# Kernel optimization log

Hardware: AMD Instinct MI355X
Metric: run time of the kernel (lower is better)

Reference implementation:

```python
import jax, jax.numpy as jnp
import numpy as np

B, T, D = 2, 2048, 2048
H, KV, DH = 16, 8, 128
N, W, K = 1024, 256, 8


def rotate_half(x):
    x1, x2 = x[..., : DH // 2], x[..., DH // 2 :]
    return jnp.concatenate((-x2, x1), axis=-1)


def setup_inputs() -> dict:
    key = jax.random.key(0)
    ks = jax.random.split(key, 10)
    hidden_states = jax.random.normal(ks[0], (B, T, D), dtype=jnp.float32)
    cos = jax.random.uniform(ks[1], (B, T, DH), dtype=jnp.float32, minval=-1.0, maxval=1.0)
    sin = jax.random.uniform(ks[2], (B, T, DH), dtype=jnp.float32, minval=-1.0, maxval=1.0)
    mem = jax.random.normal(ks[3], (B, N, D), dtype=jnp.float32)
    Wq = jax.random.normal(ks[4], (D, D), dtype=jnp.float32) * 0.02
    Wk = jax.random.normal(ks[5], (KV * DH, D), dtype=jnp.float32) * 0.02
    Wv = jax.random.normal(ks[6], (KV * DH, D), dtype=jnp.float32) * 0.02
    Wo = jax.random.normal(ks[7], (D, D), dtype=jnp.float32) * 0.02
    Wg = jnp.zeros((1, D), dtype=jnp.float32)          # module inits gate weight to zeros
    bg = jnp.full((1,), 2.0, dtype=jnp.float32)        # and gate bias to 2.0
    return dict(hidden_states=hidden_states, cos=cos, sin=sin, mem=mem,
                Wq=Wq, Wk=Wk, Wv=Wv, Wo=Wo, Wg=Wg, bg=bg)


def reference(hidden_states, cos, sin, mem, Wq, Wk, Wv, Wo, Wg, bg):
    scale = DH ** -0.5
    n_rep = H // KV
    # projections -> [B, heads, T, d_h]
    q = (hidden_states @ Wq.T).reshape(B, T, H, DH).transpose(0, 2, 1, 3)
    k = (hidden_states @ Wk.T).reshape(B, T, KV, DH).transpose(0, 2, 1, 3)
    v = (hidden_states @ Wv.T).reshape(B, T, KV, DH).transpose(0, 2, 1, 3)
    # rotary (cos/sin are [B,T,d_h] -> broadcast over heads)
    c, s = cos[:, None], sin[:, None]
    q = q * c + rotate_half(q) * s
    k = k * c + rotate_half(k) * s
    # GQA repeat kv heads
    k_local = jnp.repeat(k, n_rep, axis=1)
    v_local = jnp.repeat(v, n_rep, axis=1)
    # --- local sliding-window causal attention (dense TxT mask, as in SDPA path) ---
    row = jnp.arange(T)[:, None]
    col = jnp.arange(T)[None, :]
    allowed = (col <= row) & (col >= row - W + 1)
    bias = jnp.where(allowed, 0.0, -jnp.inf).astype(q.dtype)
    scores = jnp.einsum('bhtd,bhsd->bhts', q, k_local) * scale + bias
    o_local = jnp.einsum('bhts,bhsd->bhtd', jax.nn.softmax(scores, axis=-1), v_local)
    o_local = o_local.transpose(0, 2, 1, 3).reshape(B, T, D) @ Wo.T
    # --- memory retrieval path (memory is detached in the original) ---
    mem_c = jax.lax.stop_gradient(mem)
    k_mem = (mem_c @ Wk.T).reshape(B, N, KV, DH).transpose(0, 2, 1, 3)
    v_mem = (mem_c @ Wv.T).reshape(B, N, KV, DH).transpose(0, 2, 1, 3)
    k_mem = jnp.repeat(k_mem, n_rep, axis=1)  # [B,H,N,d_h]
    v_mem = jnp.repeat(v_mem, n_rep, axis=1)
    q_chunk = q.mean(axis=2)                  # [B,H,d_h]
    sim_chunk = jnp.einsum('bhd,bhnd->bhn', q_chunk, k_mem) * scale
    _, idx = jax.lax.top_k(sim_chunk, K)      # [B,H,K]
    k_sh = jnp.take_along_axis(k_mem, idx[..., None], axis=2)  # [B,H,K,d_h]
    v_sh = jnp.take_along_axis(v_mem, idx[..., None], axis=2)
    sim_tok = jnp.einsum('bhtd,bhkd->bhtk', q, k_sh) * scale
    o_mem = jnp.einsum('bhtk,bhkd->bhtd', jax.nn.softmax(sim_tok, axis=-1), v_sh)
    o_mem = o_mem.transpose(0, 2, 1, 3).reshape(B, T, D)
    # --- learned gate fusion ---
    g = jax.nn.sigmoid(hidden_states @ Wg.T + bg)  # [B,T,1]
    return g * o_local + (1.0 - g) * o_mem
```

## Files before the change

kernel.cpp:

```cpp
#include <hip/hip_runtime.h>
#include <stdint.h>

#define B_   2
#define T_   2048
#define D_   2048
#define H_   16
#define KV_  8
#define DH_  128
#define NMEM 1024
#define WWIN 256
#define KSEL 8
#define BT   (B_*T_)
#define KVSTR 2048
#define QKVSTR 4096

__constant__ const float kScale = 0.08838834764831845f;

typedef __attribute__((ext_vector_type(8))) short s16x8;
typedef __attribute__((ext_vector_type(4))) float f32x4;

__device__ inline unsigned short f2bf(float f) {
  union { float f; unsigned int u; } c; c.f = f;
  unsigned int u = c.u;
  unsigned int r = u + 0x7fffu + ((u >> 16) & 1u);
  return (unsigned short)(r >> 16);
}
__device__ inline float bf2f(unsigned short v) {
  union { unsigned int u; float f; } c; c.u = ((unsigned int)v) << 16;
  return c.f;
}
__device__ inline f32x4 fzero4() { f32x4 v; v[0]=0.f; v[1]=0.f; v[2]=0.f; v[3]=0.f; return v; }

__global__ __launch_bounds__(256) void conv_kernel(const float* __restrict__ src,
                                                   unsigned short* __restrict__ dst, int n) {
  int i = blockIdx.x * 256 + threadIdx.x;
  if (i * 4 >= n) return;
  float4 v = ((const float4*)src)[i];
  uint2 o;
  o.x = (unsigned)f2bf(v.x) | ((unsigned)f2bf(v.y) << 16);
  o.y = (unsigned)f2bf(v.z) | ((unsigned)f2bf(v.w) << 16);
  ((uint2*)dst)[i] = o;
}

#define AOFF(buf, half) ((buf)*32768 + (half)*16384)
#define BOFF(buf, half) (65536 + (buf)*32768 + (half)*16384)

#define PH_MFMA(P, BF) \
  { \
    _Pragma("unroll") \
    for (int mi = 0; mi < 2; ++mi) { \
      _Pragma("unroll") \
      for (int ni = 0; ni < 4; ++ni) { \
        acc[P][mi][ni] = __builtin_amdgcn_mfma_f32_16x16x32_bf16(af[mi][0], BF[ni][0], acc[P][mi][ni], 0, 0, 0); \
        acc[P][mi][ni] = __builtin_amdgcn_mfma_f32_16x16x32_bf16(af[mi][1], BF[ni][1], acc[P][mi][ni], 0, 0, 0); \
      } \
    } \
  }

template<int MODE>
__global__ __launch_bounds__(512, 2) void gemm256(const unsigned short* __restrict__ A,
                                                  const unsigned short* __restrict__ Bw,
                                                  int N, int K, int lda, int ldc,
                                                  unsigned short* __restrict__ Cb,
                                                  const float* __restrict__ g,
                                                  const unsigned short* __restrict__ omem,
                                                  float* __restrict__ dout) {
  __shared__ __align__(16) char lds[131072];
  const int tid = threadIdx.x;
  const int wv = tid >> 6, lane = tid & 63;
  const int l15 = lane & 15, lg = lane >> 4;
  const int wr = wv >> 1, wc = wv & 1;
  const int gx = gridDim.x;
  const int nwg = gx * gridDim.y;
  const int flat = blockIdx.y * gx + blockIdx.x;
  const int chunk = nwg >> 3;
  const int wg = (flat & 7) * chunk + (flat >> 3);
  const int bx = wg % gx, by = wg / gx;
  const int m0 = by * 256, n0 = bx * 256;
  const int NT = K >> 6;

  auto stage_half = [&](const unsigned short* base, int stride, int row0, int koff, int ldsoff) {
#pragma unroll
    for (int ld = 0; ld < 2; ++ld) {
      int s = ld * 512 + tid;
      int row = s >> 3, cs = s & 7;
      int cg = cs ^ (row & 7);
      const unsigned short* src = base + (size_t)(row0 + row) * stride + koff + cg * 8;
      __builtin_amdgcn_global_load_lds((const __attribute__((address_space(1))) void*)src,
          (__attribute__((address_space(3))) void*)(lds + ldsoff + ld * 8192 + wv * 1024), 16, 0, 0);
    }
  };
  auto rdA = [&](int buf, int half, int mi, int kk) -> s16x8 {
    int r = wr * 32 + mi * 16 + l15;
    int slot = (kk * 4 + lg) ^ (r & 7);
    return *(const s16x8*)(lds + AOFF(buf, half) + r * 128 + slot * 16);
  };
  auto rdB = [&](int buf, int half, int ni, int kk) -> s16x8 {
    int r = wc * 64 + ni * 16 + l15;
    int slot = (kk * 4 + lg) ^ (r & 7);
    return *(const s16x8*)(lds + BOFF(buf, half) + r * 128 + slot * 16);
  };

  f32x4 acc[4][2][4];
#pragma unroll
  for (int p = 0; p < 4; ++p)
#pragma unroll
    for (int mi = 0; mi < 2; ++mi)
#pragma unroll
      for (int ni = 0; ni < 4; ++ni) acc[p][mi][ni] = fzero4();

  stage_half(A,  lda, m0,       0,  AOFF(0, 0));
  stage_half(Bw, K,   n0,       0,  BOFF(0, 0));
  stage_half(A,  lda, m0 + 128, 0,  AOFF(0, 1));
  stage_half(Bw, K,   n0 + 128, 0,  BOFF(0, 1));
  stage_half(A,  lda, m0,       64, AOFF(1, 0));
  stage_half(Bw, K,   n0,       64, BOFF(1, 0));
  stage_half(A,  lda, m0 + 128, 64, AOFF(1, 1));
  asm volatile("s_waitcnt vmcnt(6)" ::: "memory");
  __builtin_amdgcn_s_barrier();

  int cur = 0;
  for (int t = 0; t < NT; ++t, cur ^= 1) {
    const int nxt = cur ^ 1;
    s16x8 af[2][2], b0f[4][2], b1f[4][2];
#pragma unroll
    for (int mi = 0; mi < 2; ++mi) {
      af[mi][0] = rdA(cur, 0, mi, 0);
      af[mi][1] = rdA(cur, 0, mi, 1);
    }
#pragma unroll
    for (int ni = 0; ni < 4; ++ni) {
      b0f[ni][0] = rdB(cur, 0, ni, 0);
      b0f[ni][1] = rdB(cur, 0, ni, 1);
    }
    if (t + 1 < NT) stage_half(Bw, K, n0 + 128, (t + 1) * 64, BOFF(nxt, 1));
    __builtin_amdgcn_s_barrier();
    asm volatile("s_waitcnt lgkmcnt(0)" ::: "memory");
    __builtin_amdgcn_s_setprio(1);
    PH_MFMA(0, b0f);
    __builtin_amdgcn_s_setprio(0);
    __builtin_amdgcn_s_barrier();
#pragma unroll
    for (int ni = 0; ni < 4; ++ni) {
      b1f[ni][0] = rdB(cur, 1, ni, 0);
      b1f[ni][1] = rdB(cur, 1, ni, 1);
    }
    if (t + 2 < NT) stage_half(A, lda, m0, (t + 2) * 64, AOFF(cur, 0));
    __builtin_amdgcn_s_barrier();
    asm volatile("s_waitcnt lgkmcnt(0)" ::: "memory");
    __builtin_amdgcn_s_setprio(1);
    PH_MFMA(1, b1f);
    __builtin_amdgcn_s_setprio(0);
    __builtin_amdgcn_s_barrier();
#pragma unroll
    for (int mi = 0; mi < 2; ++mi) {
      af[mi][0] = rdA(cur, 1, mi, 0);
      af[mi][1] = rdA(cur, 1, mi, 1);
    }
    if (t + 2 < NT) stage_half(Bw, K, n0, (t + 2) * 64, BOFF(cur, 0));
    __builtin_amdgcn_s_barrier();
    asm volatile("s_waitcnt lgkmcnt(0)" ::: "memory");
    __builtin_amdgcn_s_setprio(1);
    PH_MFMA(2, b0f);
    __builtin_amdgcn_s_setprio(0);
    __builtin_amdgcn_s_barrier();
    if (t + 2 < NT) stage_half(A, lda, m0 + 128, (t + 2) * 64, AOFF(cur, 1));
    __builtin_amdgcn_s_barrier();
    asm volatile("s_waitcnt lgkmcnt(0)" ::: "memory");
    __builtin_amdgcn_s_setprio(1);
    PH_MFMA(3, b1f);
    __builtin_amdgcn_s_setprio(0);
    if (t < NT - 2) asm volatile("s_waitcnt vmcnt(6)" ::: "memory");
    else            asm volatile("s_waitcnt vmcnt(0)" ::: "memory");
    __builtin_amdgcn_s_barrier();
  }

#pragma unroll
  for (int p = 0; p < 4; ++p)
#pragma unroll
    for (int mi = 0; mi < 2; ++mi)
#pragma unroll
      for (int ni = 0; ni < 4; ++ni)
#pragma unroll
        for (int j = 0; j < 4; ++j) {
          int row_g = m0 + (p >> 1) * 128 + wr * 32 + mi * 16 + lg * 4 + j;
          int col_g = n0 + (p & 1) * 128 + wc * 64 + ni * 16 + l15;
          float v = acc[p][mi][ni][j];
          size_t o = (size_t)row_g * ldc + col_g;
          if constexpr (MODE == 0) {
            Cb[o] = f2bf(v);
          } else {
            float gv = g[row_g];
            dout[o] = gv * v + (1.f - gv) * bf2f(omem[o]);
          }
        }
}

#define B2OFF(buf) (65536 + (buf)*16384)

__global__ __launch_bounds__(512, 2) void gemm256n(const unsigned short* __restrict__ A,
                                                   const unsigned short* __restrict__ Bw,
                                                   int N, int K, int lda, int ldc,
                                                   const float* __restrict__ g,
                                                   const unsigned short* __restrict__ omem,
                                                   float* __restrict__ dout) {
  __shared__ __align__(16) char lds[98304];
  const int tid = threadIdx.x;
  const int wv = tid >> 6, lane = tid & 63;
  const int l15 = lane & 15, lg = lane >> 4;
  const int wr = wv >> 1, wc = wv & 1;
  const int gx = gridDim.x;
  const int nwg = gx * gridDim.y;
  const int flat = blockIdx.y * gx + blockIdx.x;
  const int chunk = nwg >> 3;
  const int wg = (flat & 7) * chunk + (flat >> 3);
  const int bx = wg % gx, by = wg / gx;
  const int m0 = by * 256, n0 = bx * 128;
  const int NT = K >> 6;

  auto stage_half = [&](const unsigned short* base, int stride, int row0, int koff, int ldsoff) {
#pragma unroll
    for (int ld = 0; ld < 2; ++ld) {
      int s = ld * 512 + tid;
      int row = s >> 3, cs = s & 7;
      int cg = cs ^ (row & 7);
      const unsigned short* src = base + (size_t)(row0 + row) * stride + koff + cg * 8;
      __builtin_amdgcn_global_load_lds((const __attribute__((address_space(1))) void*)src,
          (__attribute__((address_space(3))) void*)(lds + ldsoff + ld * 8192 + wv * 1024), 16, 0, 0);
    }
  };
  auto rdA = [&](int buf, int half, int mi, int kk) -> s16x8 {
    int r = wr * 32 + mi * 16 + l15;
    int slot = (kk * 4 + lg) ^ (r & 7);
    return *(const s16x8*)(lds + AOFF(buf, half) + r * 128 + slot * 16);
  };
  auto rdB = [&](int buf, int ni, int kk) -> s16x8 {
    int r = wc * 64 + ni * 16 + l15;
    int slot = (kk * 4 + lg) ^ (r & 7);
    return *(const s16x8*)(lds + B2OFF(buf) + r * 128 + slot * 16);
  };

  f32x4 acc[2][2][4];
#pragma unroll
  for (int p = 0; p < 2; ++p)
#pragma unroll
    for (int mi = 0; mi < 2; ++mi)
#pragma unroll
      for (int ni = 0; ni < 4; ++ni) acc[p][mi][ni] = fzero4();

  stage_half(A,  lda, m0,       0,  AOFF(0, 0));
  stage_half(Bw, K,   n0,       0,  B2OFF(0));
  stage_half(A,  lda, m0 + 128, 0,  AOFF(0, 1));
  stage_half(A,  lda, m0,       64, AOFF(1, 0));
  stage_half(Bw, K,   n0,       64, B2OFF(1));
  asm volatile("s_waitcnt vmcnt(4)" ::: "memory");
  __builtin_amdgcn_s_barrier();

  int cur = 0;
  for (int t = 0; t < NT; ++t, cur ^= 1) {
    const int nxt = cur ^ 1;
    s16x8 af[2][2], b0f[4][2];
#pragma unroll
    for (int mi = 0; mi < 2; ++mi) {
      af[mi][0] = rdA(cur, 0, mi, 0);
      af[mi][1] = rdA(cur, 0, mi, 1);
    }
#pragma unroll
    for (int ni = 0; ni < 4; ++ni) {
      b0f[ni][0] = rdB(cur, ni, 0);
      b0f[ni][1] = rdB(cur, ni, 1);
    }
    if (t + 1 < NT) stage_half(A, lda, m0 + 128, (t + 1) * 64, AOFF(nxt, 1));
    __builtin_amdgcn_s_barrier();
    asm volatile("s_waitcnt lgkmcnt(0)" ::: "memory");
    __builtin_amdgcn_s_setprio(1);
    PH_MFMA(0, b0f);
    __builtin_amdgcn_s_setprio(0);
    __builtin_amdgcn_s_barrier();
#pragma unroll
    for (int mi = 0; mi < 2; ++mi) {
      af[mi][0] = rdA(cur, 1, mi, 0);
      af[mi][1] = rdA(cur, 1, mi, 1);
    }
    if (t + 2 < NT) {
      stage_half(A,  lda, m0, (t + 2) * 64, AOFF(cur, 0));
      stage_half(Bw, K,   n0, (t + 2) * 64, B2OFF(cur));
    }
    __builtin_amdgcn_s_barrier();
    asm volatile("s_waitcnt lgkmcnt(0)" ::: "memory");
    __builtin_amdgcn_s_setprio(1);
    PH_MFMA(1, b0f);
    __builtin_amdgcn_s_setprio(0);
    if (t < NT - 2) asm volatile("s_waitcnt vmcnt(4)" ::: "memory");
    else            asm volatile("s_waitcnt vmcnt(0)" ::: "memory");
    __builtin_amdgcn_s_barrier();
  }

#pragma unroll
  for (int p = 0; p < 2; ++p)
#pragma unroll
    for (int mi = 0; mi < 2; ++mi)
#pragma unroll
      for (int ni = 0; ni < 4; ++ni)
#pragma unroll
        for (int j = 0; j < 4; ++j) {
          int row_g = m0 + p * 128 + wr * 32 + mi * 16 + lg * 4 + j;
          int col_g = n0 + wc * 64 + ni * 16 + l15;
          float v = acc[p][mi][ni][j];
          size_t o = (size_t)row_g * ldc + col_g;
          float gv = g[row_g];
          dout[o] = gv * v + (1.f - gv) * bf2f(omem[o]);
        }
}

template<int MODE>
__global__ __launch_bounds__(256) void gemm_bt(const unsigned short* __restrict__ A,
                                               const unsigned short* __restrict__ Bw,
                                               int N, int K, int lda, int ldc,
                                               unsigned short* __restrict__ Cb,
                                               const float* __restrict__ g,
                                               const unsigned short* __restrict__ omem,
                                               float* __restrict__ dout) {
  __shared__ __align__(16) unsigned short sA[128 * 32];
  __shared__ __align__(16) unsigned short sB[128 * 32];
  const int tid = threadIdx.x;
  const int wv = tid >> 6, lane = tid & 63;
  const int gx = gridDim.x;
  const int nwg = gx * gridDim.y;
  const int flat = blockIdx.y * gx + blockIdx.x;
  const int chunk = nwg >> 3;
  const int wg = (flat & 7) * chunk + (flat >> 3);
  const int bx = wg % gx, by = wg / gx;
  const int m0 = by * 128, n0 = bx * 128;
  const int wr = wv >> 1, wc = wv & 1;
  const int l15 = lane & 15, lg = lane >> 4;
  const int rowA = tid >> 2;
  const int colB = (tid & 3) * 16;
  f32x4 acc[4][4];
#pragma unroll
  for (int mi = 0; mi < 4; ++mi)
#pragma unroll
    for (int ni = 0; ni < 4; ++ni) acc[mi][ni] = fzero4();

  char* sAc = (char*)sA;
  char* sBc = (char*)sB;
  for (int k0 = 0; k0 < K; k0 += 32) {
#pragma unroll
    for (int e = 0; e < 2; ++e) {
      const char* ga = (const char*)(A + ((size_t)(m0 + rowA + e * 64) * lda + k0)) + colB;
      __builtin_amdgcn_global_load_lds((const __attribute__((address_space(1))) void*)ga,
          (__attribute__((address_space(3))) void*)(sAc + e * 4096 + wv * 1024), 16, 0, 0);
      const char* gb = (const char*)(Bw + ((size_t)(n0 + rowA + e * 64) * K + k0)) + colB;
      __builtin_amdgcn_global_load_lds((const __attribute__((address_space(1))) void*)gb,
          (__attribute__((address_space(3))) void*)(sBc + e * 4096 + wv * 1024), 16, 0, 0);
    }
    __syncthreads();
    s16x8 af[4], bf_[4];
#pragma unroll
    for (int mi = 0; mi < 4; ++mi)
      af[mi] = *(const s16x8*)&sA[(wr * 64 + mi * 16 + l15) * 32 + lg * 8];
#pragma unroll
    for (int ni = 0; ni < 4; ++ni)
      bf_[ni] = *(const s16x8*)&sB[(wc * 64 + ni * 16 + l15) * 32 + lg * 8];
#pragma unroll
    for (int mi = 0; mi < 4; ++mi)
#pragma unroll
      for (int ni = 0; ni < 4; ++ni)
        acc[mi][ni] = __builtin_amdgcn_mfma_f32_16x16x32_bf16(af[mi], bf_[ni], acc[mi][ni], 0, 0, 0);
    __syncthreads();
  }
#pragma unroll
  for (int mi = 0; mi < 4; ++mi)
#pragma unroll
    for (int ni = 0; ni < 4; ++ni)
#pragma unroll
      for (int j = 0; j < 4; ++j) {
        int row_g = m0 + wr * 64 + mi * 16 + lg * 4 + j;
        int col_g = n0 + wc * 64 + ni * 16 + l15;
        float v = acc[mi][ni][j];
        size_t o = (size_t)row_g * ldc + col_g;
        if constexpr (MODE == 0) {
          Cb[o] = f2bf(v);
        } else {
          float gv = g[row_g];
          float om = bf2f(omem[o]);
          dout[o] = gv * v + (1.f - gv) * om;
        }
      }
}

__global__ __launch_bounds__(256) void rope_ip_kernel(unsigned short* __restrict__ buf,
                                                      const float* __restrict__ cosp,
                                                      const float* __restrict__ sinp,
                                                      int logp, int stride, int nthreads) {
  int i = blockIdx.x * 256 + threadIdx.x;
  if (i >= nthreads) return;
  int pp = i * 8;
  int row = pp >> logp;
  int p0 = pp & ((1 << logp) - 1);
  int blk = p0 >> 6, dd0 = p0 & 63;
  int b = row >> 11, t = row & 2047;
  const float* cb = cosp + ((size_t)b * T_ + t) * DH_;
  const float* sb = sinp + ((size_t)b * T_ + t) * DH_;
  unsigned short* p1 = buf + (size_t)row * stride + blk * 128 + dd0;
  s16x8 a = *(s16x8*)p1;
  s16x8 b8 = *(s16x8*)(p1 + 64);
  s16x8 o1, o2;
#pragma unroll
  for (int e = 0; e < 8; ++e) {
    float c1 = cb[dd0 + e], s1 = sb[dd0 + e];
    float c2 = cb[dd0 + 64 + e], s2 = sb[dd0 + 64 + e];
    float x1 = bf2f((unsigned short)a[e]), x2 = bf2f((unsigned short)b8[e]);
    o1[e] = (short)f2bf(x1 * c1 - x2 * s1);
    o2[e] = (short)f2bf(x2 * c2 + x1 * s2);
  }
  *(s16x8*)p1 = o1;
  *(s16x8*)(p1 + 64) = o2;
}

__global__ __launch_bounds__(256) void cs_kernel(const float* __restrict__ hs,
                                                 const float* __restrict__ cosp,
                                                 const float* __restrict__ sinp,
                                                 float* __restrict__ Cp, float* __restrict__ Sp) {
  __shared__ __align__(16) float hsL[32][128];
  __shared__ __align__(16) float csL[32][32];
  __shared__ __align__(16) float snL[32][32];
  const int tid = threadIdx.x;
  const int j0 = blockIdx.x * 128, d0 = blockIdx.y * 32;
  const int b = blockIdx.z >> 3, sp = blockIdx.z & 7;
  const int dq = (tid & 7) * 4;
  const int jq = (tid >> 3) * 4;
  float4 aC[4], aS[4];
#pragma unroll
  for (int a = 0; a < 4; ++a) {
    aC[a] = make_float4(0.f, 0.f, 0.f, 0.f);
    aS[a] = make_float4(0.f, 0.f, 0.f, 0.f);
  }
  const int csrow = tid >> 3, csc4 = tid & 7;
  for (int tile = 0; tile < 8; ++tile) {
    int t0 = sp * 256 + tile * 32;
    const float4* hs4 = (const float4*)(hs + ((size_t)b * T_ + t0) * D_ + j0);
#pragma unroll
    for (int r = 0; r < 4; ++r) {
      int i = tid + r * 256;
      int row = i >> 5, c4 = i & 31;
      *(float4*)&hsL[row][c4 * 4] = hs4[(size_t)row * (D_ / 4) + c4];
    }
    const float4* cp4 = (const float4*)(cosp + ((size_t)b * T_ + t0) * DH_ + d0);
    const float4* sp4 = (const float4*)(sinp + ((size_t)b * T_ + t0) * DH_ + d0);
    *(float4*)&csL[csrow][csc4 * 4] = cp4[(size_t)csrow * (DH_ / 4) + csc4];
    *(float4*)&snL[csrow][csc4 * 4] = sp4[(size_t)csrow * (DH_ / 4) + csc4];
    __syncthreads();
#pragma unroll 8
    for (int tt = 0; tt < 32; ++tt) {
      float4 cv = *(const float4*)&csL[tt][dq];
      float4 sv = *(const float4*)&snL[tt][dq];
      float4 hv = *(const float4*)&hsL[tt][jq];
      float ca[4] = {cv.x, cv.y, cv.z, cv.w};
      float sa[4] = {sv.x, sv.y, sv.z, sv.w};
#pragma unroll
      for (int a = 0; a < 4; ++a) {
        aC[a].x += ca[a] * hv.x; aC[a].y += ca[a] * hv.y;
        aC[a].z += ca[a] * hv.z; aC[a].w += ca[a] * hv.w;
        aS[a].x += sa[a] * hv.x; aS[a].y += sa[a] * hv.y;
        aS[a].z += sa[a] * hv.z; aS[a].w += sa[a] * hv.w;
      }
    }
    __syncthreads();
  }
#pragma unroll
  for (int a = 0; a < 4; ++a) {
    size_t o = ((size_t)(sp * B_ + b) * DH_ + d0 + dq + a) * D_ + j0 + jq;
    *(float4*)&Cp[o] = aC[a];
    *(float4*)&Sp[o] = aS[a];
  }
}

__global__ __launch_bounds__(256) void reduce_cs_kernel(const float4* __restrict__ Cp,
                                                        const float4* __restrict__ Sp,
                                                        float4* __restrict__ Cr,
                                                        float4* __restrict__ Sr) {
  int i = blockIdx.x * 256 + threadIdx.x;
  const int str = (B_ * DH_ * D_) / 4;
  float4 c = Cp[i], s = Sp[i];
#pragma unroll
  for (int p = 1; p < 8; ++p) {
    float4 cp = Cp[i + (size_t)p * str], sq = Sp[i + (size_t)p * str];
    c.x += cp.x; c.y += cp.y; c.z += cp.z; c.w += cp.w;
    s.x += sq.x; s.y += sq.y; s.z += sq.z; s.w += sq.w;
  }
  Cr[i] = c; Sr[i] = s;
}

__global__ __launch_bounds__(256) void qchunk_kernel(const float* __restrict__ Wq,
                                                     const float* __restrict__ Cr,
                                                     const float* __restrict__ Sr,
                                                     float* __restrict__ qc) {
  int gid = blockIdx.x * 256 + threadIdx.x;
  int wid = gid >> 6, lane = gid & 63;
  int b = wid >> 11, rem = wid & 2047;
  int h = rem >> 7, d = rem & 127;
  const float* w1 = Wq + (size_t)(h * DH_ + d) * D_;
  int dp = (d < 64) ? d + 64 : d - 64;
  float sgn = (d < 64) ? -1.f : 1.f;
  const float* w2 = Wq + (size_t)(h * DH_ + dp) * D_;
  const float* crow = Cr + ((size_t)b * DH_ + d) * D_;
  const float* srow = Sr + ((size_t)b * DH_ + d) * D_;
  float a1 = 0.f, a2 = 0.f;
  for (int j = lane; j < D_; j += 64) { a1 += w1[j] * crow[j]; a2 += w2[j] * srow[j]; }
#pragma unroll
  for (int off = 1; off < 64; off <<= 1) { a1 += __shfl_xor(a1, off); a2 += __shfl_xor(a2, off); }
  if (lane == 0) qc[wid] = (a1 + sgn * a2) * (1.f / (float)T_);
}

__global__ __launch_bounds__(256) void zk_kernel(const float* __restrict__ qc,
                                                 const float* __restrict__ Wk,
                                                 float* __restrict__ z) {
  int j = blockIdx.x * 256 + threadIdx.x;
  int h = blockIdx.y, b = blockIdx.z;
  int kvh = h >> 1;
  const float* qcl = qc + ((size_t)b * H_ + h) * DH_;
  const float* wb = Wk + (size_t)kvh * DH_ * D_ + j;
  float acc = 0.f;
#pragma unroll 8
  for (int d = 0; d < 128; ++d) acc += qcl[d] * wb[(size_t)d * D_];
  z[((size_t)b * H_ + h) * D_ + j] = acc;
}

__global__ __launch_bounds__(256) void sim_kernel(const float* __restrict__ z,
                                                  const float* __restrict__ mem,
                                                  float* __restrict__ sim) {
  __shared__ float4 mL[16 * 512];
  int tid = threadIdx.x;
  int n0 = blockIdx.x * 16, b = blockIdx.y;
  const float4* mem4 = (const float4*)(mem + (size_t)b * NMEM * D_);
#pragma unroll
  for (int c = 0; c < 32; ++c) {
    int i = tid + c * 256;
    int r = i >> 9, j4 = i & 511;
    mL[r * 512 + (j4 ^ (r & 7))] = mem4[(size_t)(n0 + r) * 512 + j4];
  }
  __syncthreads();
  int h = tid >> 4, n = tid & 15;
  const float4* zr = (const float4*)(z + ((size_t)b * H_ + h) * D_);
  float acc = 0.f;
  for (int j4 = 0; j4 < 512; ++j4) {
    float4 zz = zr[j4];
    float4 mm = mL[n * 512 + (j4 ^ (n & 7))];
    acc += zz.x * mm.x + zz.y * mm.y + zz.z * mm.z + zz.w * mm.w;
  }
  sim[((size_t)b * H_ + h) * NMEM + n0 + n] = acc * kScale;
}

__global__ __launch_bounds__(256) void topk_kernel(const float* __restrict__ sim,
                                                   int* __restrict__ idx) {
  __shared__ float sL[1024];
  __shared__ float rv[256];
  __shared__ int ri[256];
  int tid = threadIdx.x;
  int h = blockIdx.x, b = blockIdx.y;
  const float* sp = sim + ((size_t)b * H_ + h) * NMEM;
#pragma unroll
  for (int r = 0; r < 4; ++r) sL[tid + r * 256] = sp[tid + r * 256];
  __syncthreads();
  for (int kk = 0; kk < 8; ++kk) {
    float bv = -INFINITY; int bi = 0x7fffffff;
#pragma unroll
    for (int r = 0; r < 4; ++r) {
      int i = tid + r * 256;
      float v = sL[i];
      if (v > bv || (v == bv && i < bi)) { bv = v; bi = i; }
    }
    rv[tid] = bv; ri[tid] = bi;
    __syncthreads();
    for (int s = 128; s > 0; s >>= 1) {
      if (tid < s) {
        float v2 = rv[tid + s]; int i2 = ri[tid + s];
        if (v2 > rv[tid] || (v2 == rv[tid] && i2 < ri[tid])) { rv[tid] = v2; ri[tid] = i2; }
      }
      __syncthreads();
    }
    if (tid == 0) { idx[((size_t)b * H_ + h) * KSEL + kk] = ri[0]; sL[ri[0]] = -INFINITY; }
    __syncthreads();
  }
}

__global__ __launch_bounds__(256) void memattn_kernel(const unsigned short* __restrict__ qbf,
                                                      const unsigned short* __restrict__ kvmem,
                                                      const int* __restrict__ idx,
                                                      unsigned short* __restrict__ omem) {
  __shared__ float kl[8][128];
  __shared__ float vl[8][128];
  __shared__ int selL[8];
  int tid = threadIdx.x;
  int b = blockIdx.z, h = blockIdx.y, t = blockIdx.x * 256 + tid;
  int kvh = h >> 1;
  if (tid < 8) selL[tid] = idx[((size_t)b * H_ + h) * KSEL + tid];
  __syncthreads();
  {
    int r = tid >> 5, c4 = (tid & 31) * 4;
    size_t rb = ((size_t)b * NMEM + selL[r]) * (size_t)KVSTR;
    ushort4 k4 = *(const ushort4*)(kvmem + rb + kvh * DH_ + c4);
    ushort4 v4 = *(const ushort4*)(kvmem + rb + KV_ * DH_ + kvh * DH_ + c4);
    kl[r][c4 + 0] = bf2f(k4.x); kl[r][c4 + 1] = bf2f(k4.y);
    kl[r][c4 + 2] = bf2f(k4.z); kl[r][c4 + 3] = bf2f(k4.w);
    vl[r][c4 + 0] = bf2f(v4.x); vl[r][c4 + 1] = bf2f(v4.y);
    vl[r][c4 + 2] = bf2f(v4.z); vl[r][c4 + 3] = bf2f(v4.w);
  }
  __syncthreads();
  float sc[8] = {0.f,0.f,0.f,0.f,0.f,0.f,0.f,0.f};
  const unsigned short* qr = qbf + (size_t)(b * T_ + t) * QKVSTR + h * DH_;
  for (int c = 0; c < 4; ++c) {
    const s16x8* qp = (const s16x8*)(qr + c * 32);
#pragma unroll
    for (int u = 0; u < 4; ++u) {
      s16x8 q8 = qp[u];
#pragma unroll
      for (int e = 0; e < 8; ++e) {
        float qv = bf2f((unsigned short)q8[e]);
        int d = c * 32 + u * 8 + e;
#pragma unroll
        for (int kk = 0; kk < 8; ++kk) sc[kk] += qv * kl[kk][d];
      }
    }
  }
  float sm[8], mx = -INFINITY;
#pragma unroll
  for (int kk = 0; kk < 8; ++kk) { sm[kk] = sc[kk] * kScale; mx = fmaxf(mx, sm[kk]); }
  float sum = 0.f;
#pragma unroll
  for (int kk = 0; kk < 8; ++kk) { sm[kk] = __expf(sm[kk] - mx); sum += sm[kk]; }
  float inv = 1.f / sum;
#pragma unroll
  for (int kk = 0; kk < 8; ++kk) sm[kk] *= inv;
  unsigned short* orow = omem + (size_t)(b * T_ + t) * D_ + h * DH_;
  for (int d = 0; d < 128; d += 4) {
    float o0 = 0.f, o1 = 0.f, o2 = 0.f, o3 = 0.f;
#pragma unroll
    for (int kk = 0; kk < 8; ++kk) {
      float w = sm[kk];
      o0 += w * vl[kk][d + 0];
      o1 += w * vl[kk][d + 1];
      o2 += w * vl[kk][d + 2];
      o3 += w * vl[kk][d + 3];
    }
    uint2 pk;
    pk.x = (unsigned)f2bf(o0) | ((unsigned)f2bf(o1) << 16);
    pk.y = (unsigned)f2bf(o2) | ((unsigned)f2bf(o3) << 16);
    *(uint2*)(orow + d) = pk;
  }
}

__global__ __launch_bounds__(256) void gate_kernel(const float* __restrict__ hs,
                                                   const float* __restrict__ Wg,
                                                   const float* __restrict__ bg,
                                                   float* __restrict__ g) {
  int gid = blockIdx.x * 256 + threadIdx.x;
  int row = gid >> 6, lane = gid & 63;
  const float4* hr = (const float4*)(hs + (size_t)row * D_);
  const float4* wg4 = (const float4*)Wg;
  float acc = 0.f;
#pragma unroll
  for (int it = 0; it < 8; ++it) {
    float4 hv = hr[lane + it * 64], wv = wg4[lane + it * 64];
    acc += hv.x * wv.x + hv.y * wv.y + hv.z * wv.z + hv.w * wv.w;
  }
#pragma unroll
  for (int off = 1; off < 64; off <<= 1) acc += __shfl_xor(acc, off);
  if (lane == 0) g[row] = 1.f / (1.f + __expf(-(acc + bg[0])));
}

__global__ __launch_bounds__(256) void localattn_kernel(const unsigned short* __restrict__ qbf,
                                                        const unsigned short* __restrict__ kbf,
                                                        const unsigned short* __restrict__ vbf,
                                                        unsigned short* __restrict__ olocal) {
  __shared__ __align__(16) unsigned short kL[2][32][128];
  __shared__ __align__(16) unsigned short vL[2][128][32];
  __shared__ __align__(16) unsigned short pl[4][16][40];
  const int tid = threadIdx.x;
  const int w = tid >> 6, lane = tid & 63;
  const int tb = blockIdx.x * 64;
  const int h = blockIdx.y, b = blockIdx.z;
  const int kvh = h >> 1;
  const int t0 = tb + w * 16;
  const int l15 = lane & 15, lg = lane >> 4;

  s16x8 qf[4];
  {
    const unsigned short* qb = qbf + ((size_t)(b * T_ + t0 + l15) * QKVSTR) + h * DH_ + lg * 8;
#pragma unroll
    for (int kb = 0; kb < 4; ++kb) qf[kb] = *(const s16x8*)(qb + kb * 32);
  }
  f32x4 of[8];
#pragma unroll
  for (int nb = 0; nb < 8; ++nb) of[nb] = fzero4();
  float m_r[4] = {-INFINITY, -INFINITY, -INFINITY, -INFINITY};
  float l_r[4] = {0.f, 0.f, 0.f, 0.f};

  int sstart = tb - (WWIN - 1);
  if (sstart < 0) sstart = 0;
  sstart &= ~31;
  const int slast = tb + 63;

  const int vk = tid & 15, vcg = tid >> 4;
  auto STAGE = [&](int buf, int s0) {
#pragma unroll
    for (int ld = 0; ld < 2; ++ld) {
      int s = ld * 256 + tid;
      int r = s >> 4, cs = s & 15;
      int cg = cs ^ (r & 7);
      const unsigned short* src = kbf + (size_t)(b * T_ + s0 + r) * QKVSTR + kvh * DH_ + cg * 8;
      __builtin_amdgcn_global_load_lds((const __attribute__((address_space(1))) void*)src,
          (__attribute__((address_space(3))) void*)((char*)&kL[buf][0][0] + ld * 4096 + w * 1024), 16, 0, 0);
    }
    {
      int r0 = 2 * vk;
      const unsigned short* vs = vbf + (size_t)(b * T_ + s0 + r0) * QKVSTR + kvh * DH_ + vcg * 8;
      s16x8 va = *(const s16x8*)vs;
      s16x8 vb2 = *(const s16x8*)(vs + QKVSTR);
      int q = vk >> 2;
      int colbase = 2 * (vk & 3);
#pragma unroll
      for (int e = 0; e < 8; ++e) {
        int c = vcg * 8 + e;
        int blk = q ^ ((c >> 2) & 3);
        unsigned int val = (unsigned int)(unsigned short)va[e] |
                           ((unsigned int)(unsigned short)vb2[e] << 16);
        *(unsigned int*)&vL[buf][c][blk * 8 + colbase] = val;
      }
    }
  };

  STAGE(0, sstart);
  int buf = 0;
  const int vp = (l15 >> 2) & 3;
  for (int s0 = sstart; s0 <= slast; s0 += 32, buf ^= 1) {
    __syncthreads();
    if (s0 + 32 <= slast) STAGE(buf ^ 1, s0 + 32);

    f32x4 sc[2];
    sc[0] = fzero4(); sc[1] = fzero4();
#pragma unroll
    for (int cb = 0; cb < 2; ++cb) {
#pragma unroll
      for (int kb = 0; kb < 4; ++kb) {
        int r = cb * 16 + l15;
        int c = kb * 4 + lg;
        s16x8 kf = *(const s16x8*)((char*)&kL[buf][0][0] + r * 256 + ((c ^ (r & 7)) * 16));
        sc[cb] = __builtin_amdgcn_mfma_f32_16x16x32_bf16(qf[kb], kf, sc[cb], 0, 0, 0);
      }
    }
    float pv[2][4];
#pragma unroll
    for (int j = 0; j < 4; ++j) {
      int t = t0 + lg * 4 + j;
      int s_a = s0 + l15, s_b = s_a + 16;
      float va = sc[0][j] * kScale;
      float vb = sc[1][j] * kScale;
      va = (s_a <= t && s_a + (WWIN - 1) >= t) ? va : -INFINITY;
      vb = (s_b <= t && s_b + (WWIN - 1) >= t) ? vb : -INFINITY;
      float mx = fmaxf(va, vb);
#pragma unroll
      for (int off = 1; off < 16; off <<= 1) mx = fmaxf(mx, __shfl_xor(mx, off));
      float mn = fmaxf(m_r[j], mx);
      float alpha, pa, pb;
      if (mn == -INFINITY) { alpha = 1.f; pa = 0.f; pb = 0.f; }
      else {
        alpha = __expf(m_r[j] - mn);
        pa = __expf(va - mn);
        pb = __expf(vb - mn);
      }
      m_r[j] = mn;
      float rs = pa + pb;
#pragma unroll
      for (int off = 1; off < 16; off <<= 1) rs += __shfl_xor(rs, off);
      l_r[j] = l_r[j] * alpha + rs;
#pragma unroll
      for (int nb = 0; nb < 8; ++nb) of[nb][j] *= alpha;
      pv[0][j] = pa; pv[1][j] = pb;
    }
#pragma unroll
    for (int cb = 0; cb < 2; ++cb)
#pragma unroll
      for (int j = 0; j < 4; ++j)
        pl[w][lg * 4 + j][cb * 16 + l15] = f2bf(pv[cb][j]);
    asm volatile("s_waitcnt lgkmcnt(0)" ::: "memory");
    __builtin_amdgcn_sched_barrier(0);
    s16x8 pa8 = *(const s16x8*)&pl[w][l15][lg * 8];
#pragma unroll
    for (int nb = 0; nb < 8; ++nb) {
      int c = nb * 16 + l15;
      s16x8 vf = *(const s16x8*)&vL[buf][c][(lg ^ vp) * 8];
      of[nb] = __builtin_amdgcn_mfma_f32_16x16x32_bf16(pa8, vf, of[nb], 0, 0, 0);
    }
  }

  float inv[4];
#pragma unroll
  for (int j = 0; j < 4; ++j) inv[j] = 1.f / l_r[j];
#pragma unroll
  for (int nb = 0; nb < 8; ++nb)
#pragma unroll
    for (int j = 0; j < 4; ++j) {
      int t = t0 + lg * 4 + j;
      olocal[(size_t)(b * T_ + t) * QKVSTR + h * DH_ + nb * 16 + l15] = f2bf(of[nb][j] * inv[j]);
    }
}

extern "C" void kernel_launch(void* const* d_in, const int* in_sizes, int n_in,
                              void* d_out, int out_size, void* d_ws, size_t ws_size,
                              hipStream_t stream) {
  const float* hs   = (const float*)d_in[0];
  const float* cosp = (const float*)d_in[1];
  const float* sinp = (const float*)d_in[2];
  const float* mem  = (const float*)d_in[3];
  const float* Wq   = (const float*)d_in[4];
  const float* Wk   = (const float*)d_in[5];
  const float* Wv   = (const float*)d_in[6];
  const float* Wo   = (const float*)d_in[7];
  const float* Wg   = (const float*)d_in[8];
  const float* bg   = (const float*)d_in[9];
  float* out = (float*)d_out;

  char* p = (char*)d_ws;
  auto alloc = [&](size_t bytes) { char* r = p; p += (bytes + 255) & ~(size_t)255; return r; };
  float* qc     = (float*)alloc((size_t)B_ * H_ * DH_ * 4);
  float* gbuf   = (float*)alloc((size_t)BT * 4);
  float* zbuf   = (float*)alloc((size_t)B_ * H_ * D_ * 4);
  float* simbuf = (float*)alloc((size_t)B_ * H_ * NMEM * 4);
  int*   idxbuf = (int*)alloc((size_t)B_ * H_ * KSEL * 4);
  unsigned short* hs_bf   = (unsigned short*)alloc((size_t)BT * D_ * 2);
  unsigned short* qkv_raw = (unsigned short*)alloc((size_t)BT * QKVSTR * 2);
  unsigned short* wbig    = (unsigned short*)alloc((size_t)2 * D_ * D_ * 2);
  unsigned short* mem_bf  = (unsigned short*)alloc((size_t)B_ * NMEM * D_ * 2);
  unsigned short* kvmem   = (unsigned short*)alloc((size_t)B_ * NMEM * KVSTR * 2);

  float* Cp = (float*)d_out;
  float* Sp = Cp + (size_t)8 * B_ * DH_ * D_;
  float* Cr = (float*)mem_bf;
  float* Sr = Cr + (size_t)B_ * DH_ * D_;
  unsigned short* omem_bf = hs_bf;

  conv_kernel<<<(BT * D_ / 4 + 255) / 256, 256, 0, stream>>>(hs, hs_bf, BT * D_);
  conv_kernel<<<(D_ * D_ / 4 + 255) / 256, 256, 0, stream>>>(Wq, wbig, D_ * D_);
  conv_kernel<<<(KV_ * DH_ * D_ / 4 + 255) / 256, 256, 0, stream>>>(Wk, wbig + (size_t)D_ * D_, KV_ * DH_ * D_);
  conv_kernel<<<(KV_ * DH_ * D_ / 4 + 255) / 256, 256, 0, stream>>>(Wv, wbig + (size_t)D_ * D_ + (size_t)KV_ * DH_ * D_, KV_ * DH_ * D_);
  gemm256<0><<<dim3(QKVSTR / 256, BT / 256), 512, 0, stream>>>(hs_bf, wbig, QKVSTR, D_, D_, QKVSTR, qkv_raw, nullptr, nullptr, nullptr);
  conv_kernel<<<(B_ * NMEM * D_ / 4 + 255) / 256, 256, 0, stream>>>(mem, mem_bf, B_ * NMEM * D_);
  gemm_bt<0><<<dim3(KVSTR / 128, (B_ * NMEM) / 128), 256, 0, stream>>>(mem_bf, wbig + (size_t)D_ * D_, KVSTR, D_, D_, KVSTR, kvmem, nullptr, nullptr, nullptr);

  rope_ip_kernel<<<(BT * D_ / 16 + 255) / 256, 256, 0, stream>>>(qkv_raw, cosp, sinp, 10, QKVSTR, BT * D_ / 16);
  rope_ip_kernel<<<(BT * KV_ * DH_ / 16 + 255) / 256, 256, 0, stream>>>(qkv_raw + D_, cosp, sinp, 9, QKVSTR, BT * KV_ * DH_ / 16);

  cs_kernel<<<dim3(D_ / 128, DH_ / 32, B_ * 8), 256, 0, stream>>>(hs, cosp, sinp, Cp, Sp);
  reduce_cs_kernel<<<(B_ * DH_ * D_ / 4) / 256, 256, 0, stream>>>((const float4*)Cp, (const float4*)Sp, (float4*)Cr, (float4*)Sr);
  qchunk_kernel<<<(B_ * H_ * DH_) / 4, 256, 0, stream>>>(Wq, Cr, Sr, qc);
  zk_kernel<<<dim3(D_ / 256, H_, B_), 256, 0, stream>>>(qc, Wk, zbuf);
  sim_kernel<<<dim3(NMEM / 16, B_), 256, 0, stream>>>(zbuf, mem, simbuf);
  topk_kernel<<<dim3(H_, B_), 256, 0, stream>>>(simbuf, idxbuf);

  memattn_kernel<<<dim3(T_ / 256, H_, B_), 256, 0, stream>>>(qkv_raw, kvmem, idxbuf, omem_bf);

  gate_kernel<<<BT / 4, 256, 0, stream>>>(hs, Wg, bg, gbuf);

  localattn_kernel<<<dim3(T_ / 64, H_, B_), 256, 0, stream>>>(qkv_raw, qkv_raw + D_, qkv_raw + D_ + KV_ * DH_, qkv_raw);

  conv_kernel<<<(D_ * D_ / 4 + 255) / 256, 256, 0, stream>>>(Wo, wbig, D_ * D_);
  gemm256n<<<dim3(D_ / 128, BT / 256), 512, 0, stream>>>(qkv_raw, wbig, D_, D_, QKVSTR, D_, gbuf, omem_bf, out);
}
```

Before: 417.1 us.

## Project only top-k selected memory rows instead of full memory K/V GEMM

Removes the full GEMM that projected every memory row into K and V, and adds a small kernel that gathers only the selected top-k memory rows per batch/head and projects them with MFMA. memattn now reads precomputed fp32 selected K/V. This avoids computing and storing projections for the many unselected memory rows. In exchange, the selection path gains a low-parallelism kernel (one block per head) that streams weights directly from global memory, and the Cr/Sr scratch gets its own buffer because mem_bf must stay live.

```diff
diff --git a/kernel.cpp b/kernel.cpp
--- a/kernel.cpp
+++ b/kernel.cpp
@@ -11,7 +11,6 @@
 #define WWIN 256
 #define KSEL 8
 #define BT   (B_*T_)
-#define KVSTR 2048
 #define QKVSTR 4096
 
 __constant__ const float kScale = 0.08838834764831845f;
@@ -313,80 +312,68 @@
         }
 }
 
-template<int MODE>
-__global__ __launch_bounds__(256) void gemm_bt(const unsigned short* __restrict__ A,
-                                               const unsigned short* __restrict__ Bw,
-                                               int N, int K, int lda, int ldc,
-                                               unsigned short* __restrict__ Cb,
-                                               const float* __restrict__ g,
-                                               const unsigned short* __restrict__ omem,
-                                               float* __restrict__ dout) {
-  __shared__ __align__(16) unsigned short sA[128 * 32];
-  __shared__ __align__(16) unsigned short sB[128 * 32];
+__global__ __launch_bounds__(256) void gsel_kernel(const unsigned short* __restrict__ mem_bf,
+                                                   const unsigned short* __restrict__ wkv,
+                                                   const int* __restrict__ idx,
+                                                   float* __restrict__ kshp,
+                                                   float* __restrict__ vshp) {
+  __shared__ __align__(16) unsigned short selA[16][2056];
+  __shared__ int selL[8];
   const int tid = threadIdx.x;
-  const int wv = tid >> 6, lane = tid & 63;
-  const int gx = gridDim.x;
-  const int nwg = gx * gridDim.y;
-  const int flat = blockIdx.y * gx + blockIdx.x;
-  const int chunk = nwg >> 3;
-  const int wg = (flat & 7) * chunk + (flat >> 3);
-  const int bx = wg % gx, by = wg / gx;
-  const int m0 = by * 128, n0 = bx * 128;
-  const int wr = wv >> 1, wc = wv & 1;
+  const int h = blockIdx.x, b = blockIdx.y;
+  const int kvh = h >> 1;
+  if (tid < 8) selL[tid] = idx[(b * H_ + h) * KSEL + tid];
+  __syncthreads();
+#pragma unroll
+  for (int it = 0; it < 8; ++it) {
+    int i = it * 256 + tid;
+    int r = i >> 8, c8 = i & 255;
+    *(s16x8*)&selA[r][c8 * 8] =
+        *(const s16x8*)(mem_bf + ((size_t)(b * NMEM + selL[r])) * D_ + c8 * 8);
+  }
+  {
+    s16x8 z = {0, 0, 0, 0, 0, 0, 0, 0};
+#pragma unroll
+    for (int it = 0; it < 8; ++it) {
+      int i = it * 256 + tid;
+      int r = 8 + (i >> 8), c8 = i & 255;
+      *(s16x8*)&selA[r][c8 * 8] = z;
+    }
+  }
+  __syncthreads();
+  const int w = tid >> 6, lane = tid & 63;
   const int l15 = lane & 15, lg = lane >> 4;
-  const int rowA = tid >> 2;
-  const int colB = (tid & 3) * 16;
-  f32x4 acc[4][4];
-#pragma unroll
-  for (int mi = 0; mi < 4; ++mi)
-#pragma unroll
-    for (int ni = 0; ni < 4; ++ni) acc[mi][ni] = fzero4();
-
-  char* sAc = (char*)sA;
-  char* sBc = (char*)sB;
-  for (int k0 = 0; k0 < K; k0 += 32) {
-#pragma unroll
-    for (int e = 0; e < 2; ++e) {
-      const char* ga = (const char*)(A + ((size_t)(m0 + rowA + e * 64) * lda + k0)) + colB;
-      __builtin_amdgcn_global_load_lds((const __attribute__((address_space(1))) void*)ga,
-          (__attribute__((address_space(3))) void*)(sAc + e * 4096 + wv * 1024), 16, 0, 0);
-      const char* gb = (const char*)(Bw + ((size_t)(n0 + rowA + e * 64) * K + k0)) + colB;
-      __builtin_amdgcn_global_load_lds((const __attribute__((address_space(1))) void*)gb,
-          (__attribute__((address_space(3))) void*)(sBc + e * 4096 + wv * 1024), 16, 0, 0);
-    }
-    __syncthreads();
-    s16x8 af[4], bf_[4];
-#pragma unroll
-    for (int mi = 0; mi < 4; ++mi)
-      af[mi] = *(const s16x8*)&sA[(wr * 64 + mi * 16 + l15) * 32 + lg * 8];
-#pragma unroll
-    for (int ni = 0; ni < 4; ++ni)
-      bf_[ni] = *(const s16x8*)&sB[(wc * 64 + ni * 16 + l15) * 32 + lg * 8];
-#pragma unroll
-    for (int mi = 0; mi < 4; ++mi)
-#pragma unroll
-      for (int ni = 0; ni < 4; ++ni)
-        acc[mi][ni] = __builtin_amdgcn_mfma_f32_16x16x32_bf16(af[mi], bf_[ni], acc[mi][ni], 0, 0, 0);
-    __syncthreads();
-  }
-#pragma unroll
-  for (int mi = 0; mi < 4; ++mi)
-#pragma unroll
-    for (int ni = 0; ni < 4; ++ni)
-#pragma unroll
-      for (int j = 0; j < 4; ++j) {
-        int row_g = m0 + wr * 64 + mi * 16 + lg * 4 + j;
-        int col_g = n0 + wc * 64 + ni * 16 + l15;
-        float v = acc[mi][ni][j];
-        size_t o = (size_t)row_g * ldc + col_g;
-        if constexpr (MODE == 0) {
-          Cb[o] = f2bf(v);
-        } else {
-          float gv = g[row_g];
-          float om = bf2f(omem[o]);
-          dout[o] = gv * v + (1.f - gv) * om;
-        }
+  f32x4 acc[4];
+#pragma unroll
+  for (int ni = 0; ni < 4; ++ni) acc[ni] = fzero4();
+  const unsigned short* brow[4];
+#pragma unroll
+  for (int ni = 0; ni < 4; ++ni) {
+    int col = w * 64 + ni * 16 + l15;
+    brow[ni] = (col < 128)
+        ? (wkv + (size_t)(kvh * DH_ + col) * D_)
+        : (wkv + (size_t)(KV_ * DH_ + kvh * DH_ + (col - 128)) * D_);
+  }
+  for (int kt = 0; kt < D_ / 32; ++kt) {
+    s16x8 af = *(const s16x8*)&selA[l15][kt * 32 + lg * 8];
+#pragma unroll
+    for (int ni = 0; ni < 4; ++ni) {
+      s16x8 bf_ = *(const s16x8*)(brow[ni] + kt * 32 + lg * 8);
+      acc[ni] = __builtin_amdgcn_mfma_f32_16x16x32_bf16(af, bf_, acc[ni], 0, 0, 0);
+    }
+  }
+#pragma unroll
+  for (int ni = 0; ni < 4; ++ni)
+#pragma unroll
+    for (int j = 0; j < 4; ++j) {
+      int row = lg * 4 + j;
+      int col = w * 64 + ni * 16 + l15;
+      if (row < 8) {
+        float* outp = (col < 128 ? kshp : vshp) +
+                      ((size_t)(b * H_ + h) * KSEL + row) * DH_ + (col & 127);
+        *outp = acc[ni][j];
       }
+    }
 }
 
 __global__ __launch_bounds__(256) void rope_ip_kernel(unsigned short* __restrict__ buf,
@@ -586,26 +573,20 @@
 }
 
 __global__ __launch_bounds__(256) void memattn_kernel(const unsigned short* __restrict__ qbf,
-                                                      const unsigned short* __restrict__ kvmem,
-                                                      const int* __restrict__ idx,
+                                                      const float* __restrict__ ksh,
+                                                      const float* __restrict__ vsh,
                                                       unsigned short* __restrict__ omem) {
   __shared__ float kl[8][128];
   __shared__ float vl[8][128];
-  __shared__ int selL[8];
   int tid = threadIdx.x;
   int b = blockIdx.z, h = blockIdx.y, t = blockIdx.x * 256 + tid;
-  int kvh = h >> 1;
-  if (tid < 8) selL[tid] = idx[((size_t)b * H_ + h) * KSEL + tid];
-  __syncthreads();
-  {
-    int r = tid >> 5, c4 = (tid & 31) * 4;
-    size_t rb = ((size_t)b * NMEM + selL[r]) * (size_t)KVSTR;
-    ushort4 k4 = *(const ushort4*)(kvmem + rb + kvh * DH_ + c4);
-    ushort4 v4 = *(const ushort4*)(kvmem + rb + KV_ * DH_ + kvh * DH_ + c4);
-    kl[r][c4 + 0] = bf2f(k4.x); kl[r][c4 + 1] = bf2f(k4.y);
-    kl[r][c4 + 2] = bf2f(k4.z); kl[r][c4 + 3] = bf2f(k4.w);
-    vl[r][c4 + 0] = bf2f(v4.x); vl[r][c4 + 1] = bf2f(v4.y);
-    vl[r][c4 + 2] = bf2f(v4.z); vl[r][c4 + 3] = bf2f(v4.w);
+  const float* ks = ksh + ((size_t)b * H_ + h) * KSEL * DH_;
+  const float* vs = vsh + ((size_t)b * H_ + h) * KSEL * DH_;
+#pragma unroll
+  for (int r = 0; r < 4; ++r) {
+    int i = tid + r * 256;
+    ((float*)kl)[i] = ks[i];
+    ((float*)vl)[i] = vs[i];
   }
   __syncthreads();
   float sc[8] = {0.f,0.f,0.f,0.f,0.f,0.f,0.f,0.f};
@@ -829,15 +810,17 @@
   float* zbuf   = (float*)alloc((size_t)B_ * H_ * D_ * 4);
   float* simbuf = (float*)alloc((size_t)B_ * H_ * NMEM * 4);
   int*   idxbuf = (int*)alloc((size_t)B_ * H_ * KSEL * 4);
+  float* ksh    = (float*)alloc((size_t)B_ * H_ * KSEL * DH_ * 4);
+  float* vsh    = (float*)alloc((size_t)B_ * H_ * KSEL * DH_ * 4);
   unsigned short* hs_bf   = (unsigned short*)alloc((size_t)BT * D_ * 2);
   unsigned short* qkv_raw = (unsigned short*)alloc((size_t)BT * QKVSTR * 2);
   unsigned short* wbig    = (unsigned short*)alloc((size_t)2 * D_ * D_ * 2);
   unsigned short* mem_bf  = (unsigned short*)alloc((size_t)B_ * NMEM * D_ * 2);
-  unsigned short* kvmem   = (unsigned short*)alloc((size_t)B_ * NMEM * KVSTR * 2);
+  float* crsr             = (float*)alloc((size_t)2 * B_ * DH_ * D_ * 4);
 
   float* Cp = (float*)d_out;
   float* Sp = Cp + (size_t)8 * B_ * DH_ * D_;
-  float* Cr = (float*)mem_bf;
+  float* Cr = crsr;
   float* Sr = Cr + (size_t)B_ * DH_ * D_;
   unsigned short* omem_bf = hs_bf;
 
@@ -847,7 +830,6 @@
   conv_kernel<<<(KV_ * DH_ * D_ / 4 + 255) / 256, 256, 0, stream>>>(Wv, wbig + (size_t)D_ * D_ + (size_t)KV_ * DH_ * D_, KV_ * DH_ * D_);
   gemm256<0><<<dim3(QKVSTR / 256, BT / 256), 512, 0, stream>>>(hs_bf, wbig, QKVSTR, D_, D_, QKVSTR, qkv_raw, nullptr, nullptr, nullptr);
   conv_kernel<<<(B_ * NMEM * D_ / 4 + 255) / 256, 256, 0, stream>>>(mem, mem_bf, B_ * NMEM * D_);
-  gemm_bt<0><<<dim3(KVSTR / 128, (B_ * NMEM) / 128), 256, 0, stream>>>(mem_bf, wbig + (size_t)D_ * D_, KVSTR, D_, D_, KVSTR, kvmem, nullptr, nullptr, nullptr);
 
   rope_ip_kernel<<<(BT * D_ / 16 + 255) / 256, 256, 0, stream>>>(qkv_raw, cosp, sinp, 10, QKVSTR, BT * D_ / 16);
   rope_ip_kernel<<<(BT * KV_ * DH_ / 16 + 255) / 256, 256, 0, stream>>>(qkv_raw + D_, cosp, sinp, 9, QKVSTR, BT * KV_ * DH_ / 16);
@@ -859,7 +841,8 @@
   sim_kernel<<<dim3(NMEM / 16, B_), 256, 0, stream>>>(zbuf, mem, simbuf);
   topk_kernel<<<dim3(H_, B_), 256, 0, stream>>>(simbuf, idxbuf);
 
-  memattn_kernel<<<dim3(T_ / 256, H_, B_), 256, 0, stream>>>(qkv_raw, kvmem, idxbuf, omem_bf);
+  gsel_kernel<<<dim3(H_, B_), 256, 0, stream>>>(mem_bf, wbig + (size_t)D_ * D_, idxbuf, ksh, vsh);
+  memattn_kernel<<<dim3(T_ / 256, H_, B_), 256, 0, stream>>>(qkv_raw, ksh, vsh, omem_bf);
 
   gate_kernel<<<BT / 4, 256, 0, stream>>>(hs, Wg, bg, gbuf);
 
```

Measured after the change: 402.2 us. 1.04x faster.
